# Kernel optimization log

Measured on AMD Instinct MI355X. Metric: run time of the kernel, lower is better.

The kernel has to match this reference:

```python
import jax, jax.numpy as jnp
import numpy as np

EPS = 1e-5
N0, K1, K2 = 1000, 500, 100  # node counts fixed by the view() calls in the source


def _conv_bn_relu(x, w, b, g, be):
    # Conv1d(k=1) == per-node linear; BatchNorm1d in training mode over nodes
    h = x @ w.T + b                      # (N, Cout)
    mu = h.mean(0)
    var = h.var(0)                       # biased variance, as torch BN uses
    return jax.nn.relu(g * (h - mu) * jax.lax.rsqrt(var + EPS) + be)


def _linear_relu(x, w, b):
    return jax.nn.relu(x @ w.T + b)


def _sag_pool(x, src, dst, ew, w_rel, w_root, bias, k):
    # SAGPooling with GraphConv scorer (sum aggregation weighted by edge_attr)
    N = x.shape[0]
    agg = jax.ops.segment_sum(ew[:, None] * x[src], dst, num_segments=N)  # (N, C)
    score = agg @ w_rel + x @ w_root + bias                               # (N,)
    top_s, perm = jax.lax.top_k(score, k)
    xk = x[perm] * jnp.tanh(top_s)[:, None]                               # (k, C)
    # re-index edges: keep only edges between surviving nodes (mask, fixed E)
    new_idx = jnp.zeros(N, jnp.int32).at[perm].set(jnp.arange(k, dtype=jnp.int32))
    keep = jnp.zeros(N, bool).at[perm].set(True)
    valid = keep[src] & keep[dst]
    nsrc = jnp.where(valid, new_idx[src], 0)
    ndst = jnp.where(valid, new_idx[dst], 0)
    new_ew = jnp.where(valid, ew, 0.0)  # zero weight == edge removed
    return xk, nsrc, ndst, new_ew


def setup_inputs() -> dict:
    key = jax.random.key(0)
    ks = jax.random.split(key, 32)
    nrm = lambda k, sh, s=0.05: jax.random.normal(k, sh, jnp.float32) * s
    E = 32000
    return {
        "x": jax.random.normal(ks[0], (1, N0, 3), jnp.float32),
        "edge_index": jax.random.randint(ks[1], (2, E), 0, N0, jnp.int32),
        "edge_attr": jax.random.uniform(ks[2], (E,), jnp.float32),
        # input: Conv1d(3,64)+BN
        "w0": nrm(ks[3], (64, 3)), "b0": jnp.zeros(64), "g0": jnp.ones(64), "be0": jnp.zeros(64),
        # mlp_first: Conv1d(64,64)+BN
        "w1": nrm(ks[4], (64, 64)), "b1": jnp.zeros(64), "g1": jnp.ones(64), "be1": jnp.zeros(64),
        # mlp_second: Conv1d(64,128)+BN, Conv1d(128,200)+BN
        "w2a": nrm(ks[5], (128, 64)), "b2a": jnp.zeros(128), "g2a": jnp.ones(128), "be2a": jnp.zeros(128),
        "w2b": nrm(ks[6], (200, 128)), "b2b": jnp.zeros(200), "g2b": jnp.ones(200), "be2b": jnp.zeros(200),
        # mlp_third: Conv1d(200,128), Conv1d(128,2) (no BN)
        "w3a": nrm(ks[7], (128, 200)), "b3a": jnp.zeros(128),
        "w3b": nrm(ks[8], (2, 128)), "b3b": jnp.zeros(2),
        # SAGPooling scorers (GraphConv(in_channels, 1))
        "p1_wrel": nrm(ks[9], (64,)), "p1_wroot": nrm(ks[10], (64,)), "p1_b": jnp.zeros(()),
        "p2_wrel": nrm(ks[11], (200,)), "p2_wroot": nrm(ks[12], (200,)), "p2_b": jnp.zeros(()),
    }


def reference(x, edge_index, edge_attr,
              w0, b0, g0, be0, w1, b1, g1, be1,
              w2a, b2a, g2a, be2a, w2b, b2b, g2b, be2b,
              w3a, b3a, w3b, b3b,
              p1_wrel, p1_wroot, p1_b, p2_wrel, p2_wroot, p2_b):
    h = x.reshape(N0, 3)
    src, dst = edge_index[0], edge_index[1]
    ew = edge_attr.reshape(-1)

    h = _conv_bn_relu(h, w0, b0, g0, be0)      # (1000, 64)
    h = _conv_bn_relu(h, w1, b1, g1, be1)      # (1000, 64)
    h, src, dst, ew = _sag_pool(h, src, dst, ew, p1_wrel, p1_wroot, p1_b, K1)

    h = _conv_bn_relu(h, w2a, b2a, g2a, be2a)  # (500, 128)
    h = _conv_bn_relu(h, w2b, b2b, g2b, be2b)  # (500, 200)
    h, src, dst, ew = _sag_pool(h, src, dst, ew, p2_wrel, p2_wroot, p2_b, K2)

    g = h.max(0)                               # global max pool over 100 nodes -> (200,)
    h3 = _linear_relu(g, w3a, b3a)             # (128,)
    out = _linear_relu(h3, w3b, b3b)           # (2,)
    return jax.nn.log_softmax(out)[None, :]    # (1, 2)
```

## Files before the change

kernel.cpp:

```cpp
#include <hip/hip_runtime.h>
#include <math.h>

#define EPS 1e-5f
#define N0 1000
#define K1 500
#define K2 100
#define NE 32000

__device__ __forceinline__ float bnr(float h, float sc, float sh) {
    float v = fmaf(h, sc, sh);
    return v > 0.f ? v : 0.f;
}

__global__ void k_lin0(const float* __restrict__ x, const float* __restrict__ w0,
                       const float* __restrict__ b0, float* __restrict__ h0,
                       float* __restrict__ psum0) {
    int t = threadIdx.x;
    int c = t & 63, ns = t >> 6;
    int nb = blockIdx.x * 128;
    float wa = w0[c * 3 + 0], wb = w0[c * 3 + 1], wc = w0[c * 3 + 2], bb = b0[c];
    float s = 0.f, q = 0.f;
    for (int j = 0; j < 32; ++j) {
        int n = nb + ns + 4 * j;
        if (n < N0) {
            float h = fmaf(wa, x[n * 3], fmaf(wb, x[n * 3 + 1], fmaf(wc, x[n * 3 + 2], bb)));
            h0[n * 64 + c] = h;
            s += h; q += h * h;
        }
    }
    __shared__ float rs[256], rq[256];
    rs[t] = s; rq[t] = q;
    __syncthreads();
    if (ns == 0) {
        psum0[blockIdx.x * 128 + c]      = rs[c] + rs[c + 64] + rs[c + 128] + rs[c + 192];
        psum0[blockIdx.x * 128 + 64 + c] = rq[c] + rq[c + 64] + rq[c + 128] + rq[c + 192];
    }
}

__global__ void k_lin1(const float* __restrict__ h0, const float* __restrict__ w1,
                       const float* __restrict__ b1v, const float* __restrict__ g0,
                       const float* __restrict__ be0, const float* __restrict__ psum0,
                       float* __restrict__ h1, float* __restrict__ psum1) {
    __shared__ float xs[64][65];
    __shared__ float wsm[64][65];
    __shared__ float sc0[64], sh0[64];
    __shared__ float rs[256], rq[256];
    int t = threadIdx.x;
    int nb = blockIdx.x * 64;
    if (t < 64) {
        float s = 0.f, q = 0.f;
        for (int i = 0; i < 8; ++i) { s += psum0[i * 128 + t]; q += psum0[i * 128 + 64 + t]; }
        float mu = s * (1.f / N0);
        float var = q * (1.f / N0) - mu * mu;
        float sc = g0[t] * rsqrtf(var + EPS);
        sc0[t] = sc; sh0[t] = be0[t] - mu * sc;
    }
    __syncthreads();
    for (int i = 0; i < 16; ++i) {
        int e = t + i * 256;
        int r = e >> 6, cc = e & 63;
        int n = nb + r;
        xs[r][cc] = (n < N0) ? bnr(h0[n * 64 + cc], sc0[cc], sh0[cc]) : 0.f;
        wsm[r][cc] = w1[e];
    }
    __syncthreads();
    int c = t & 63, ns = t >> 6;
    float s = 0.f, q = 0.f;
    for (int j = 0; j < 16; ++j) {
        int ln = ns + 4 * j;
        int n = nb + ln;
        if (n < N0) {
            float acc = b1v[c];
            #pragma unroll
            for (int k = 0; k < 64; ++k) acc = fmaf(xs[ln][k], wsm[c][k], acc);
            h1[n * 64 + c] = acc;
            s += acc; q += acc * acc;
        }
    }
    rs[t] = s; rq[t] = q;
    __syncthreads();
    if (ns == 0) {
        psum1[blockIdx.x * 128 + c]      = rs[c] + rs[c + 64] + rs[c + 128] + rs[c + 192];
        psum1[blockIdx.x * 128 + 64 + c] = rq[c] + rq[c + 64] + rq[c + 128] + rq[c + 192];
    }
}

__global__ void k_score1(const float* __restrict__ h1, const float* __restrict__ psum1,
                         const float* __restrict__ g1, const float* __restrict__ be1,
                         const float* __restrict__ wrel, const float* __restrict__ wroot,
                         const float* __restrict__ pb,
                         float* __restrict__ t1, float* __restrict__ sc1) {
    __shared__ float sc[64], sh[64];
    int t = threadIdx.x;
    if (t < 64) {
        float s = 0.f, q = 0.f;
        for (int i = 0; i < 16; ++i) { s += psum1[i * 128 + t]; q += psum1[i * 128 + 64 + t]; }
        float mu = s * (1.f / N0);
        float var = q * (1.f / N0) - mu * mu;
        float sv = g1[t] * rsqrtf(var + EPS);
        sc[t] = sv; sh[t] = be1[t] - mu * sv;
    }
    __syncthreads();
    int lane = t & 63, w = t >> 6;
    int n = blockIdx.x * 4 + w;
    if (n < N0) {
        float v = bnr(h1[n * 64 + lane], sc[lane], sh[lane]);
        float dr = v * wrel[lane], dt = v * wroot[lane];
        #pragma unroll
        for (int m = 32; m >= 1; m >>= 1) {
            dr += __shfl_xor(dr, m, 64);
            dt += __shfl_xor(dt, m, 64);
        }
        if (lane == 0) { t1[n] = dr; sc1[n] = dt + pb[0]; }
    }
}

__global__ void k_scatter1(const int* __restrict__ ei, const float* __restrict__ ea,
                           const float* __restrict__ t1, float* __restrict__ sc1) {
    __shared__ float acc[N0];
    int t = threadIdx.x;
    for (int i = t; i < N0; i += 256) acc[i] = 0.f;
    __syncthreads();
    for (int e = blockIdx.x * 256 + t; e < NE; e += gridDim.x * 256) {
        float w = ea[e];
        if (w != 0.f) atomicAdd(&acc[ei[NE + e]], w * t1[ei[e]]);
    }
    __syncthreads();
    for (int i = t; i < N0; i += 256) {
        float v = acc[i];
        if (v != 0.f) atomicAdd(&sc1[i], v);
    }
}

__global__ void k_rank1(const float* __restrict__ sc1, const float* __restrict__ h1,
                        const float* __restrict__ psum1, const float* __restrict__ g1,
                        const float* __restrict__ be1,
                        float* __restrict__ xp1, int* __restrict__ keep, int* __restrict__ nidx) {
    __shared__ float ss[N0];
    __shared__ float sc[64], sh[64];
    int t = threadIdx.x;
    if (t < 64) {
        float s = 0.f, q = 0.f;
        for (int i = 0; i < 16; ++i) { s += psum1[i * 128 + t]; q += psum1[i * 128 + 64 + t]; }
        float mu = s * (1.f / N0);
        float var = q * (1.f / N0) - mu * mu;
        float sv = g1[t] * rsqrtf(var + EPS);
        sc[t] = sv; sh[t] = be1[t] - mu * sv;
    }
    for (int i = t; i < N0; i += 256) ss[i] = sc1[i];
    __syncthreads();
    int lane = t & 63, w = t >> 6;
    int n = blockIdx.x * 4 + w;
    if (n < N0) {
        float s = ss[n];
        int r = 0;
        for (int m = lane; m < N0; m += 64) {
            float sm = ss[m];
            r += (sm > s) || (sm == s && m < n);
        }
        #pragma unroll
        for (int msk = 32; msk >= 1; msk >>= 1) r += __shfl_xor(r, msk, 64);
        if (lane == 0) { keep[n] = (r < K1) ? 1 : 0; nidx[n] = (r < K1) ? r : 0; }
        if (r < K1) {
            float tn = tanhf(s);
            xp1[r * 64 + lane] = bnr(h1[n * 64 + lane], sc[lane], sh[lane]) * tn;
        }
    }
}

__global__ void k_lin2a_remap(const float* __restrict__ xp1, const float* __restrict__ w2a,
                              const float* __restrict__ b2a, float* __restrict__ h2a,
                              float* __restrict__ psum2a,
                              const int* __restrict__ ei, const float* __restrict__ ea,
                              const int* __restrict__ keep, const int* __restrict__ nidx,
                              int* __restrict__ nsrc, int* __restrict__ ndst,
                              float* __restrict__ new_ew) {
    __shared__ float xs[64][65];
    __shared__ float wsm[128][65];
    __shared__ float rs[256], rq[256];
    int b = blockIdx.x;
    int t = threadIdx.x;
    if (b < 8) {
        int nb = b * 64;
        for (int i = 0; i < 16; ++i) {
            int e = t + i * 256;
            int r = e >> 6, cc = e & 63;
            int n = nb + r;
            xs[r][cc] = (n < K1) ? xp1[n * 64 + cc] : 0.f;
        }
        for (int i = 0; i < 32; ++i) {
            int e = t + i * 256;
            wsm[e >> 6][e & 63] = w2a[e];
        }
        __syncthreads();
        int c = t & 127, ns = t >> 7;
        float s = 0.f, q = 0.f;
        for (int j = 0; j < 32; ++j) {
            int ln = ns + 2 * j;
            int n = nb + ln;
            if (n < K1) {
                float acc = b2a[c];
                #pragma unroll
                for (int k = 0; k < 64; ++k) acc = fmaf(xs[ln][k], wsm[c][k], acc);
                h2a[n * 128 + c] = acc;
                s += acc; q += acc * acc;
            }
        }
        rs[t] = s; rq[t] = q;
        __syncthreads();
        if (ns == 0) {
            psum2a[b * 256 + c]       = rs[c] + rs[c + 128];
            psum2a[b * 256 + 128 + c] = rq[c] + rq[c + 128];
        }
    } else {
        int e = (b - 8) * 256 + t;
        if (e < NE) {
            int s = ei[e], d = ei[NE + e];
            bool v = keep[s] && keep[d];
            nsrc[e] = v ? nidx[s] : 0;
            ndst[e] = v ? nidx[d] : 0;
            new_ew[e] = v ? ea[e] : 0.f;
        }
    }
}

__global__ void k_lin2b(const float* __restrict__ h2a, const float* __restrict__ psum2a,
                        const float* __restrict__ g2a, const float* __restrict__ be2a,
                        const float* __restrict__ w2b, const float* __restrict__ b2b,
                        float* __restrict__ h2b, float* __restrict__ psum2b) {
    __shared__ float wsm[200][33];
    __shared__ float xs[25][33];
    __shared__ float sc[128], sh[128];
    int t = threadIdx.x;
    if (t < 128) {
        float s = 0.f, q = 0.f;
        for (int i = 0; i < 8; ++i) { s += psum2a[i * 256 + t]; q += psum2a[i * 256 + 128 + t]; }
        float mu = s * (1.f / K1);
        float var = q * (1.f / K1) - mu * mu;
        float sv = g2a[t] * rsqrtf(var + EPS);
        sc[t] = sv; sh[t] = be2a[t] - mu * sv;
    }
    __syncthreads();
    int nb = blockIdx.x * 25;
    float acc[25];
    if (t < 200) {
        float bb = b2b[t];
        #pragma unroll
        for (int r = 0; r < 25; ++r) acc[r] = bb;
    }
    for (int kt = 0; kt < 4; ++kt) {
        int k0 = kt * 32;
        __syncthreads();
        for (int e = t; e < 200 * 32; e += 256) {
            int r = e >> 5, k = e & 31;
            wsm[r][k] = w2b[r * 128 + k0 + k];
        }
        for (int e = t; e < 25 * 32; e += 256) {
            int r = e >> 5, k = e & 31;
            int n = nb + r;
            xs[r][k] = bnr(h2a[n * 128 + k0 + k], sc[k0 + k], sh[k0 + k]);
        }
        __syncthreads();
        if (t < 200) {
            for (int k = 0; k < 32; ++k) {
                float wv = wsm[t][k];
                #pragma unroll
                for (int r = 0; r < 25; ++r) acc[r] = fmaf(xs[r][k], wv, acc[r]);
            }
        }
    }
    if (t < 200) {
        float s = 0.f, q = 0.f;
        #pragma unroll
        for (int r = 0; r < 25; ++r) {
            int n = nb + r;
            h2b[n * 200 + t] = acc[r];
            s += acc[r]; q += acc[r] * acc[r];
        }
        psum2b[blockIdx.x * 400 + t]       = s;
        psum2b[blockIdx.x * 400 + 200 + t] = q;
    }
}

__global__ void k_score2(const float* __restrict__ h2b, const float* __restrict__ psum2b,
                         const float* __restrict__ g2b, const float* __restrict__ be2b,
                         const float* __restrict__ wrel, const float* __restrict__ wroot,
                         const float* __restrict__ pb,
                         float* __restrict__ t2, float* __restrict__ sc2) {
    __shared__ float sc[200], sh[200];
    int t = threadIdx.x;
    if (t < 200) {
        float s = 0.f, q = 0.f;
        for (int i = 0; i < 20; ++i) { s += psum2b[i * 400 + t]; q += psum2b[i * 400 + 200 + t]; }
        float mu = s * (1.f / K1);
        float var = q * (1.f / K1) - mu * mu;
        float sv = g2b[t] * rsqrtf(var + EPS);
        sc[t] = sv; sh[t] = be2b[t] - mu * sv;
    }
    __syncthreads();
    int lane = t & 63, w = t >> 6;
    int n = blockIdx.x * 4 + w;
    if (n < K1) {
        float dr = 0.f, dt = 0.f;
        #pragma unroll
        for (int j = 0; j < 4; ++j) {
            int ch = lane + 64 * j;
            if (ch < 200) {
                float v = bnr(h2b[n * 200 + ch], sc[ch], sh[ch]);
                dr = fmaf(v, wrel[ch], dr);
                dt = fmaf(v, wroot[ch], dt);
            }
        }
        #pragma unroll
        for (int m = 32; m >= 1; m >>= 1) {
            dr += __shfl_xor(dr, m, 64);
            dt += __shfl_xor(dt, m, 64);
        }
        if (lane == 0) { t2[n] = dr; sc2[n] = dt + pb[0]; }
    }
}

__global__ void k_scatter2(const int* __restrict__ nsrc, const int* __restrict__ ndst,
                           const float* __restrict__ new_ew, const float* __restrict__ t2,
                           float* __restrict__ sc2) {
    __shared__ float acc[K1];
    int t = threadIdx.x;
    for (int i = t; i < K1; i += 256) acc[i] = 0.f;
    __syncthreads();
    for (int e = blockIdx.x * 256 + t; e < NE; e += gridDim.x * 256) {
        float w = new_ew[e];
        if (w != 0.f) atomicAdd(&acc[ndst[e]], w * t2[nsrc[e]]);
    }
    __syncthreads();
    for (int i = t; i < K1; i += 256) {
        float v = acc[i];
        if (v != 0.f) atomicAdd(&sc2[i], v);
    }
}

__global__ void k_rank2(const float* __restrict__ sc2v, const float* __restrict__ h2b,
                        const float* __restrict__ psum2b, const float* __restrict__ g2b,
                        const float* __restrict__ be2b, float* __restrict__ xp2) {
    __shared__ float ss[K1];
    __shared__ float sc[200], sh[200];
    int t = threadIdx.x;
    if (t < 200) {
        float s = 0.f, q = 0.f;
        for (int i = 0; i < 20; ++i) { s += psum2b[i * 400 + t]; q += psum2b[i * 400 + 200 + t]; }
        float mu = s * (1.f / K1);
        float var = q * (1.f / K1) - mu * mu;
        float sv = g2b[t] * rsqrtf(var + EPS);
        sc[t] = sv; sh[t] = be2b[t] - mu * sv;
    }
    for (int i = t; i < K1; i += 256) ss[i] = sc2v[i];
    __syncthreads();
    int lane = t & 63, w = t >> 6;
    int n = blockIdx.x * 4 + w;
    if (n < K1) {
        float s = ss[n];
        int r = 0;
        for (int m = lane; m < K1; m += 64) {
            float sm = ss[m];
            r += (sm > s) || (sm == s && m < n);
        }
        #pragma unroll
        for (int msk = 32; msk >= 1; msk >>= 1) r += __shfl_xor(r, msk, 64);
        if (r < K2) {
            float tn = tanhf(s);
            #pragma unroll
            for (int j = 0; j < 4; ++j) {
                int ch = lane + 64 * j;
                if (ch < 200)
                    xp2[r * 200 + ch] = bnr(h2b[n * 200 + ch], sc[ch], sh[ch]) * tn;
            }
        }
    }
}

__global__ void k_final(const float* __restrict__ xp2, const float* __restrict__ w3a,
                        const float* __restrict__ b3a, const float* __restrict__ w3b,
                        const float* __restrict__ b3b, float* __restrict__ out) {
    __shared__ float g[200];
    __shared__ float buf[64][201];
    __shared__ float part[256];
    __shared__ float h3[128];
    __shared__ float o[2];
    int t = threadIdx.x;
    if (t < 200) {
        float m = -1e30f;
        for (int n = 0; n < K2; ++n) m = fmaxf(m, xp2[n * 200 + t]);
        g[t] = m;
    }
    __syncthreads();
    int lane = t & 63, q = t >> 6;
    for (int chunk = 0; chunk < 2; ++chunk) {
        int r0 = chunk * 64;
        __syncthreads();
        for (int e = t; e < 64 * 200; e += 256) {
            int r = e / 200, j = e - r * 200;
            buf[r][j] = w3a[r0 * 200 + e];
        }
        __syncthreads();
        float p = 0.f;
        for (int j = q * 50; j < q * 50 + 50; ++j) p = fmaf(buf[lane][j], g[j], p);
        part[t] = p;
        __syncthreads();
        if (t < 64) {
            float a = part[t] + part[t + 64] + part[t + 128] + part[t + 192] + b3a[r0 + t];
            h3[r0 + t] = fmaxf(a, 0.f);
        }
    }
    __syncthreads();
    if (t < 128) {
        int ow = t >> 6;
        float p = w3b[ow * 128 + lane] * h3[lane] + w3b[ow * 128 + 64 + lane] * h3[64 + lane];
        #pragma unroll
        for (int m = 32; m >= 1; m >>= 1) p += __shfl_xor(p, m, 64);
        if (lane == 0) o[ow] = fmaxf(p + b3b[ow], 0.f);
    }
    __syncthreads();
    if (t == 0) {
        float m = fmaxf(o[0], o[1]);
        float l = m + logf(expf(o[0] - m) + expf(o[1] - m));
        out[0] = o[0] - l;
        out[1] = o[1] - l;
    }
}

extern "C" void kernel_launch(void* const* d_in, const int* in_sizes, int n_in,
                              void* d_out, int out_size, void* d_ws, size_t ws_size,
                              hipStream_t stream) {
    const float* x    = (const float*)d_in[0];
    const int*   ei   = (const int*)d_in[1];
    const float* ea   = (const float*)d_in[2];
    const float* w0   = (const float*)d_in[3];
    const float* b0   = (const float*)d_in[4];
    const float* g0   = (const float*)d_in[5];
    const float* be0  = (const float*)d_in[6];
    const float* w1   = (const float*)d_in[7];
    const float* b1   = (const float*)d_in[8];
    const float* g1   = (const float*)d_in[9];
    const float* be1  = (const float*)d_in[10];
    const float* w2a  = (const float*)d_in[11];
    const float* b2a  = (const float*)d_in[12];
    const float* g2a  = (const float*)d_in[13];
    const float* be2a = (const float*)d_in[14];
    const float* w2b  = (const float*)d_in[15];
    const float* b2b  = (const float*)d_in[16];
    const float* g2b  = (const float*)d_in[17];
    const float* be2b = (const float*)d_in[18];
    const float* w3a  = (const float*)d_in[19];
    const float* b3a  = (const float*)d_in[20];
    const float* w3b  = (const float*)d_in[21];
    const float* b3b  = (const float*)d_in[22];
    const float* p1_wrel  = (const float*)d_in[23];
    const float* p1_wroot = (const float*)d_in[24];
    const float* p1_b     = (const float*)d_in[25];
    const float* p2_wrel  = (const float*)d_in[26];
    const float* p2_wroot = (const float*)d_in[27];
    const float* p2_b     = (const float*)d_in[28];

    float* ws = (float*)d_ws;
    float* h0     = ws;
    float* h1     = ws + 64000;
    float* psum0  = ws + 128000;
    float* psum1  = ws + 129024;
    float* psum2a = ws + 131072;
    float* psum2b = ws + 133120;
    float* t1     = ws + 141120;
    float* sc1    = ws + 142120;
    float* xp1    = ws + 143120;
    float* h2a    = ws + 175120;
    float* h2b    = ws + 239120;
    float* t2     = ws + 339120;
    float* sc2    = ws + 339620;
    float* xp2    = ws + 340120;
    int*   keep   = (int*)(ws + 360120);
    int*   nidx   = (int*)(ws + 361120);
    int*   nsrc   = (int*)(ws + 362120);
    int*   ndst   = (int*)(ws + 394120);
    float* new_ew = ws + 426120;

    float* out = (float*)d_out;

    k_lin0<<<8, 256, 0, stream>>>(x, w0, b0, h0, psum0);
    k_lin1<<<16, 256, 0, stream>>>(h0, w1, b1, g0, be0, psum0, h1, psum1);
    k_score1<<<250, 256, 0, stream>>>(h1, psum1, g1, be1, p1_wrel, p1_wroot, p1_b, t1, sc1);
    k_scatter1<<<16, 256, 0, stream>>>(ei, ea, t1, sc1);
    k_rank1<<<250, 256, 0, stream>>>(sc1, h1, psum1, g1, be1, xp1, keep, nidx);
    k_lin2a_remap<<<133, 256, 0, stream>>>(xp1, w2a, b2a, h2a, psum2a,
                                           ei, ea, keep, nidx, nsrc, ndst, new_ew);
    k_lin2b<<<20, 256, 0, stream>>>(h2a, psum2a, g2a, be2a, w2b, b2b, h2b, psum2b);
    k_score2<<<125, 256, 0, stream>>>(h2b, psum2b, g2b, be2b, p2_wrel, p2_wroot, p2_b, t2, sc2);
    k_scatter2<<<16, 256, 0, stream>>>(nsrc, ndst, new_ew, t2, sc2);
    k_rank2<<<125, 256, 0, stream>>>(sc2, h2b, psum2b, g2b, be2b, xp2);
    k_final<<<1, 256, 0, stream>>>(xp2, w3a, b3a, w3b, b3b, out);
}
```

Baseline: 130.3 us.

## Fuse all stages into one persistent kernel with software grid barriers

Replaces eleven separate kernel launches with a pre-clear kernel plus one persistent 64-block kernel. The stages are separated by an atomic generation-counter grid barrier, which is meant to remove per-launch overhead and the gaps between launches. BatchNorm partial sums now go into global accumulators through atomicAdd instead of per-block partial arrays. In exchange, each stage runs on at most 64 blocks, so wide stages like scoring and ranking lose parallelism. The spin barrier also relies on all 64 blocks being resident at the same time.

Result: slower. 171.7 us (+31.8%).

```diff
diff --git a/kernel.cpp b/kernel.cpp
--- a/kernel.cpp
+++ b/kernel.cpp
@@ -6,191 +6,206 @@
 #define K1 500
 #define K2 100
 #define NE 32000
+#define NB 64
 
 __device__ __forceinline__ float bnr(float h, float sc, float sh) {
     float v = fmaf(h, sc, sh);
     return v > 0.f ? v : 0.f;
 }
 
-__global__ void k_lin0(const float* __restrict__ x, const float* __restrict__ w0,
-                       const float* __restrict__ b0, float* __restrict__ h0,
-                       float* __restrict__ psum0) {
+struct Args {
+    const float *x; const int *ei; const float *ea;
+    const float *w0, *b0, *g0, *be0;
+    const float *w1, *b1, *g1, *be1;
+    const float *w2a, *b2a, *g2a, *be2a;
+    const float *w2b, *b2b, *g2b, *be2b;
+    const float *w3a, *b3a, *w3b, *b3b;
+    const float *p1_wrel, *p1_wroot, *p1_b, *p2_wrel, *p2_wroot, *p2_b;
+    float *h0, *h1, *sums0, *sums1, *sums2a, *sums2b;
+    float *t1, *sc1, *xp1, *h2a, *h2b, *t2, *sc2, *xp2;
+    int *keep, *nidx, *nsrc, *ndst; float *new_ew;
+    unsigned *bar, *gen;
+    float *out;
+};
+
+__device__ __forceinline__ void gsync(unsigned* bar, unsigned* gen) {
+    __syncthreads();
+    if (threadIdx.x == 0) {
+        unsigned g = __hip_atomic_load(gen, __ATOMIC_RELAXED, __HIP_MEMORY_SCOPE_AGENT);
+        unsigned a = __hip_atomic_fetch_add(bar, 1u, __ATOMIC_ACQ_REL, __HIP_MEMORY_SCOPE_AGENT);
+        if (a == NB - 1) {
+            __hip_atomic_store(bar, 0u, __ATOMIC_RELAXED, __HIP_MEMORY_SCOPE_AGENT);
+            __hip_atomic_fetch_add(gen, 1u, __ATOMIC_ACQ_REL, __HIP_MEMORY_SCOPE_AGENT);
+        } else {
+            while (__hip_atomic_load(gen, __ATOMIC_ACQUIRE, __HIP_MEMORY_SCOPE_AGENT) == g) {
+                __builtin_amdgcn_s_sleep(1);
+            }
+        }
+        __threadfence();
+    }
+    __syncthreads();
+}
+
+__global__ void k_pre(float* sums, unsigned* bar, unsigned* gen) {
     int t = threadIdx.x;
-    int c = t & 63, ns = t >> 6;
-    int nb = blockIdx.x * 128;
-    float wa = w0[c * 3 + 0], wb = w0[c * 3 + 1], wc = w0[c * 3 + 2], bb = b0[c];
-    float s = 0.f, q = 0.f;
-    for (int j = 0; j < 32; ++j) {
-        int n = nb + ns + 4 * j;
-        if (n < N0) {
-            float h = fmaf(wa, x[n * 3], fmaf(wb, x[n * 3 + 1], fmaf(wc, x[n * 3 + 2], bb)));
-            h0[n * 64 + c] = h;
-            s += h; q += h * h;
-        }
-    }
-    __shared__ float rs[256], rq[256];
-    rs[t] = s; rq[t] = q;
-    __syncthreads();
-    if (ns == 0) {
-        psum0[blockIdx.x * 128 + c]      = rs[c] + rs[c + 64] + rs[c + 128] + rs[c + 192];
-        psum0[blockIdx.x * 128 + 64 + c] = rq[c] + rq[c + 64] + rq[c + 128] + rq[c + 192];
-    }
+    for (int i = t; i < 912; i += 256) sums[i] = 0.f;
+    if (t == 0) { *bar = 0u; *gen = 0u; }
 }
 
-__global__ void k_lin1(const float* __restrict__ h0, const float* __restrict__ w1,
-                       const float* __restrict__ b1v, const float* __restrict__ g0,
-                       const float* __restrict__ be0, const float* __restrict__ psum0,
-                       float* __restrict__ h1, float* __restrict__ psum1) {
-    __shared__ float xs[64][65];
-    __shared__ float wsm[64][65];
-    __shared__ float sc0[64], sh0[64];
-    __shared__ float rs[256], rq[256];
-    int t = threadIdx.x;
-    int nb = blockIdx.x * 64;
-    if (t < 64) {
+__global__ __launch_bounds__(256) void k_mega(Args a) {
+    union SMem {
+        struct { float xs[64][65], wsm[128][65], rs[256], rq[256], sc[64], sh[64]; } mm;
+        struct { float wsm[200][33], xs[10][33], sc[128], sh[128]; } l2b;
+        struct { float acc[N0]; } sct;
+        struct { float ss[N0], sc[200], sh[200]; } rk;
+        struct { float sc[200], sh[200]; } bn;
+        struct { float g[200], h3[128], o[2]; } fin;
+    };
+    __shared__ SMem sm;
+    const int b = blockIdx.x, t = threadIdx.x;
+    const int lane = t & 63, wv = t >> 6;
+
+    if (b < 8) {
+        int c = lane, ns = wv;
+        int nb = b * 128;
+        float wa = a.w0[c * 3], wb = a.w0[c * 3 + 1], wc = a.w0[c * 3 + 2], bb = a.b0[c];
         float s = 0.f, q = 0.f;
-        for (int i = 0; i < 8; ++i) { s += psum0[i * 128 + t]; q += psum0[i * 128 + 64 + t]; }
-        float mu = s * (1.f / N0);
-        float var = q * (1.f / N0) - mu * mu;
-        float sc = g0[t] * rsqrtf(var + EPS);
-        sc0[t] = sc; sh0[t] = be0[t] - mu * sc;
-    }
-    __syncthreads();
-    for (int i = 0; i < 16; ++i) {
-        int e = t + i * 256;
-        int r = e >> 6, cc = e & 63;
-        int n = nb + r;
-        xs[r][cc] = (n < N0) ? bnr(h0[n * 64 + cc], sc0[cc], sh0[cc]) : 0.f;
-        wsm[r][cc] = w1[e];
-    }
-    __syncthreads();
-    int c = t & 63, ns = t >> 6;
-    float s = 0.f, q = 0.f;
-    for (int j = 0; j < 16; ++j) {
-        int ln = ns + 4 * j;
-        int n = nb + ln;
-        if (n < N0) {
-            float acc = b1v[c];
-            #pragma unroll
-            for (int k = 0; k < 64; ++k) acc = fmaf(xs[ln][k], wsm[c][k], acc);
-            h1[n * 64 + c] = acc;
-            s += acc; q += acc * acc;
-        }
-    }
-    rs[t] = s; rq[t] = q;
-    __syncthreads();
-    if (ns == 0) {
-        psum1[blockIdx.x * 128 + c]      = rs[c] + rs[c + 64] + rs[c + 128] + rs[c + 192];
-        psum1[blockIdx.x * 128 + 64 + c] = rq[c] + rq[c + 64] + rq[c + 128] + rq[c + 192];
-    }
-}
-
-__global__ void k_score1(const float* __restrict__ h1, const float* __restrict__ psum1,
-                         const float* __restrict__ g1, const float* __restrict__ be1,
-                         const float* __restrict__ wrel, const float* __restrict__ wroot,
-                         const float* __restrict__ pb,
-                         float* __restrict__ t1, float* __restrict__ sc1) {
-    __shared__ float sc[64], sh[64];
-    int t = threadIdx.x;
-    if (t < 64) {
+        for (int j = 0; j < 32; ++j) {
+            int n = nb + ns + 4 * j;
+            if (n < N0) {
+                float h = fmaf(wa, a.x[n * 3], fmaf(wb, a.x[n * 3 + 1], fmaf(wc, a.x[n * 3 + 2], bb)));
+                a.h0[n * 64 + c] = h;
+                s += h; q += h * h;
+            }
+        }
+        sm.mm.rs[t] = s; sm.mm.rq[t] = q;
+        __syncthreads();
+        if (ns == 0) {
+            atomicAdd(&a.sums0[c],      sm.mm.rs[c] + sm.mm.rs[c + 64] + sm.mm.rs[c + 128] + sm.mm.rs[c + 192]);
+            atomicAdd(&a.sums0[64 + c], sm.mm.rq[c] + sm.mm.rq[c + 64] + sm.mm.rq[c + 128] + sm.mm.rq[c + 192]);
+        }
+    }
+    gsync(a.bar, a.gen);
+
+    if (b < 16) {
+        int nb = b * 64;
+        if (t < 64) {
+            float mu = a.sums0[t] * (1.f / N0);
+            float var = a.sums0[64 + t] * (1.f / N0) - mu * mu;
+            float s = a.g0[t] * rsqrtf(var + EPS);
+            sm.mm.sc[t] = s; sm.mm.sh[t] = a.be0[t] - mu * s;
+        }
+        __syncthreads();
+        for (int i = 0; i < 16; ++i) {
+            int e = t + i * 256;
+            int r = e >> 6, cc = e & 63;
+            int n = nb + r;
+            sm.mm.xs[r][cc] = (n < N0) ? bnr(a.h0[n * 64 + cc], sm.mm.sc[cc], sm.mm.sh[cc]) : 0.f;
+            sm.mm.wsm[r][cc] = a.w1[e];
+        }
+        __syncthreads();
+        int c = lane, ns = wv;
         float s = 0.f, q = 0.f;
-        for (int i = 0; i < 16; ++i) { s += psum1[i * 128 + t]; q += psum1[i * 128 + 64 + t]; }
-        float mu = s * (1.f / N0);
-        float var = q * (1.f / N0) - mu * mu;
-        float sv = g1[t] * rsqrtf(var + EPS);
-        sc[t] = sv; sh[t] = be1[t] - mu * sv;
-    }
-    __syncthreads();
-    int lane = t & 63, w = t >> 6;
-    int n = blockIdx.x * 4 + w;
-    if (n < N0) {
-        float v = bnr(h1[n * 64 + lane], sc[lane], sh[lane]);
-        float dr = v * wrel[lane], dt = v * wroot[lane];
-        #pragma unroll
-        for (int m = 32; m >= 1; m >>= 1) {
-            dr += __shfl_xor(dr, m, 64);
-            dt += __shfl_xor(dt, m, 64);
-        }
-        if (lane == 0) { t1[n] = dr; sc1[n] = dt + pb[0]; }
-    }
-}
-
-__global__ void k_scatter1(const int* __restrict__ ei, const float* __restrict__ ea,
-                           const float* __restrict__ t1, float* __restrict__ sc1) {
-    __shared__ float acc[N0];
-    int t = threadIdx.x;
-    for (int i = t; i < N0; i += 256) acc[i] = 0.f;
-    __syncthreads();
-    for (int e = blockIdx.x * 256 + t; e < NE; e += gridDim.x * 256) {
-        float w = ea[e];
-        if (w != 0.f) atomicAdd(&acc[ei[NE + e]], w * t1[ei[e]]);
-    }
-    __syncthreads();
-    for (int i = t; i < N0; i += 256) {
-        float v = acc[i];
-        if (v != 0.f) atomicAdd(&sc1[i], v);
-    }
-}
-
-__global__ void k_rank1(const float* __restrict__ sc1, const float* __restrict__ h1,
-                        const float* __restrict__ psum1, const float* __restrict__ g1,
-                        const float* __restrict__ be1,
-                        float* __restrict__ xp1, int* __restrict__ keep, int* __restrict__ nidx) {
-    __shared__ float ss[N0];
-    __shared__ float sc[64], sh[64];
-    int t = threadIdx.x;
-    if (t < 64) {
-        float s = 0.f, q = 0.f;
-        for (int i = 0; i < 16; ++i) { s += psum1[i * 128 + t]; q += psum1[i * 128 + 64 + t]; }
-        float mu = s * (1.f / N0);
-        float var = q * (1.f / N0) - mu * mu;
-        float sv = g1[t] * rsqrtf(var + EPS);
-        sc[t] = sv; sh[t] = be1[t] - mu * sv;
-    }
-    for (int i = t; i < N0; i += 256) ss[i] = sc1[i];
-    __syncthreads();
-    int lane = t & 63, w = t >> 6;
-    int n = blockIdx.x * 4 + w;
-    if (n < N0) {
-        float s = ss[n];
-        int r = 0;
-        for (int m = lane; m < N0; m += 64) {
-            float sm = ss[m];
-            r += (sm > s) || (sm == s && m < n);
-        }
-        #pragma unroll
-        for (int msk = 32; msk >= 1; msk >>= 1) r += __shfl_xor(r, msk, 64);
-        if (lane == 0) { keep[n] = (r < K1) ? 1 : 0; nidx[n] = (r < K1) ? r : 0; }
-        if (r < K1) {
-            float tn = tanhf(s);
-            xp1[r * 64 + lane] = bnr(h1[n * 64 + lane], sc[lane], sh[lane]) * tn;
-        }
-    }
-}
-
-__global__ void k_lin2a_remap(const float* __restrict__ xp1, const float* __restrict__ w2a,
-                              const float* __restrict__ b2a, float* __restrict__ h2a,
-                              float* __restrict__ psum2a,
-                              const int* __restrict__ ei, const float* __restrict__ ea,
-                              const int* __restrict__ keep, const int* __restrict__ nidx,
-                              int* __restrict__ nsrc, int* __restrict__ ndst,
-                              float* __restrict__ new_ew) {
-    __shared__ float xs[64][65];
-    __shared__ float wsm[128][65];
-    __shared__ float rs[256], rq[256];
-    int b = blockIdx.x;
-    int t = threadIdx.x;
+        for (int j = 0; j < 16; ++j) {
+            int ln = ns + 4 * j;
+            int n = nb + ln;
+            if (n < N0) {
+                float acc = a.b1[c];
+                #pragma unroll
+                for (int k = 0; k < 64; ++k) acc = fmaf(sm.mm.xs[ln][k], sm.mm.wsm[c][k], acc);
+                a.h1[n * 64 + c] = acc;
+                s += acc; q += acc * acc;
+            }
+        }
+        sm.mm.rs[t] = s; sm.mm.rq[t] = q;
+        __syncthreads();
+        if (ns == 0) {
+            atomicAdd(&a.sums1[c],      sm.mm.rs[c] + sm.mm.rs[c + 64] + sm.mm.rs[c + 128] + sm.mm.rs[c + 192]);
+            atomicAdd(&a.sums1[64 + c], sm.mm.rq[c] + sm.mm.rq[c + 64] + sm.mm.rq[c + 128] + sm.mm.rq[c + 192]);
+        }
+    }
+    gsync(a.bar, a.gen);
+
+    if (b * 16 < N0) {
+        if (t < 64) {
+            float mu = a.sums1[t] * (1.f / N0);
+            float var = a.sums1[64 + t] * (1.f / N0) - mu * mu;
+            float sv = a.g1[t] * rsqrtf(var + EPS);
+            sm.bn.sc[t] = sv; sm.bn.sh[t] = a.be1[t] - mu * sv;
+        }
+        __syncthreads();
+        for (int it = 0; it < 4; ++it) {
+            int n = b * 16 + it * 4 + wv;
+            if (n < N0) {
+                float v = bnr(a.h1[n * 64 + lane], sm.bn.sc[lane], sm.bn.sh[lane]);
+                float dr = v * a.p1_wrel[lane], dt = v * a.p1_wroot[lane];
+                #pragma unroll
+                for (int m = 32; m >= 1; m >>= 1) {
+                    dr += __shfl_xor(dr, m, 64);
+                    dt += __shfl_xor(dt, m, 64);
+                }
+                if (lane == 0) { a.t1[n] = dr; a.sc1[n] = dt + a.p1_b[0]; }
+            }
+        }
+    }
+    gsync(a.bar, a.gen);
+
+    if (b < 16) {
+        for (int i = t; i < N0; i += 256) sm.sct.acc[i] = 0.f;
+        __syncthreads();
+        for (int e = b * 256 + t; e < NE; e += 16 * 256) {
+            float w = a.ea[e];
+            if (w != 0.f) atomicAdd(&sm.sct.acc[a.ei[NE + e]], w * a.t1[a.ei[e]]);
+        }
+        __syncthreads();
+        for (int i = t; i < N0; i += 256) {
+            float v = sm.sct.acc[i];
+            if (v != 0.f) atomicAdd(&a.sc1[i], v);
+        }
+    }
+    gsync(a.bar, a.gen);
+
+    if (b * 16 < N0) {
+        if (t < 64) {
+            float mu = a.sums1[t] * (1.f / N0);
+            float var = a.sums1[64 + t] * (1.f / N0) - mu * mu;
+            float sv = a.g1[t] * rsqrtf(var + EPS);
+            sm.rk.sc[t] = sv; sm.rk.sh[t] = a.be1[t] - mu * sv;
+        }
+        for (int i = t; i < N0; i += 256) sm.rk.ss[i] = a.sc1[i];
+        __syncthreads();
+        for (int it = 0; it < 4; ++it) {
+            int n = b * 16 + it * 4 + wv;
+            if (n < N0) {
+                float s = sm.rk.ss[n];
+                int r = 0;
+                for (int m = lane; m < N0; m += 64) {
+                    float smv = sm.rk.ss[m];
+                    r += (smv > s) || (smv == s && m < n);
+                }
+                #pragma unroll
+                for (int msk = 32; msk >= 1; msk >>= 1) r += __shfl_xor(r, msk, 64);
+                if (lane == 0) { a.keep[n] = (r < K1) ? 1 : 0; a.nidx[n] = (r < K1) ? r : 0; }
+                if (r < K1) {
+                    float tn = tanhf(s);
+                    a.xp1[r * 64 + lane] = bnr(a.h1[n * 64 + lane], sm.rk.sc[lane], sm.rk.sh[lane]) * tn;
+                }
+            }
+        }
+    }
+    gsync(a.bar, a.gen);
+
     if (b < 8) {
         int nb = b * 64;
         for (int i = 0; i < 16; ++i) {
             int e = t + i * 256;
             int r = e >> 6, cc = e & 63;
             int n = nb + r;
-            xs[r][cc] = (n < K1) ? xp1[n * 64 + cc] : 0.f;
+            sm.mm.xs[r][cc] = (n < K1) ? a.xp1[n * 64 + cc] : 0.f;
         }
         for (int i = 0; i < 32; ++i) {
             int e = t + i * 256;
-            wsm[e >> 6][e & 63] = w2a[e];
+            sm.mm.wsm[e >> 6][e & 63] = a.w2a[e];
         }
         __syncthreads();
         int c = t & 127, ns = t >> 7;
@@ -199,300 +214,249 @@
             int ln = ns + 2 * j;
             int n = nb + ln;
             if (n < K1) {
-                float acc = b2a[c];
-                #pragma unroll
-                for (int k = 0; k < 64; ++k) acc = fmaf(xs[ln][k], wsm[c][k], acc);
-                h2a[n * 128 + c] = acc;
+                float acc = a.b2a[c];
+                #pragma unroll
+                for (int k = 0; k < 64; ++k) acc = fmaf(sm.mm.xs[ln][k], sm.mm.wsm[c][k], acc);
+                a.h2a[n * 128 + c] = acc;
                 s += acc; q += acc * acc;
             }
         }
-        rs[t] = s; rq[t] = q;
+        sm.mm.rs[t] = s; sm.mm.rq[t] = q;
         __syncthreads();
         if (ns == 0) {
-            psum2a[b * 256 + c]       = rs[c] + rs[c + 128];
-            psum2a[b * 256 + 128 + c] = rq[c] + rq[c + 128];
+            atomicAdd(&a.sums2a[c],       sm.mm.rs[c] + sm.mm.rs[c + 128]);
+            atomicAdd(&a.sums2a[128 + c], sm.mm.rq[c] + sm.mm.rq[c + 128]);
         }
     } else {
-        int e = (b - 8) * 256 + t;
-        if (e < NE) {
-            int s = ei[e], d = ei[NE + e];
-            bool v = keep[s] && keep[d];
-            nsrc[e] = v ? nidx[s] : 0;
-            ndst[e] = v ? nidx[d] : 0;
-            new_ew[e] = v ? ea[e] : 0.f;
-        }
-    }
-}
-
-__global__ void k_lin2b(const float* __restrict__ h2a, const float* __restrict__ psum2a,
-                        const float* __restrict__ g2a, const float* __restrict__ be2a,
-                        const float* __restrict__ w2b, const float* __restrict__ b2b,
-                        float* __restrict__ h2b, float* __restrict__ psum2b) {
-    __shared__ float wsm[200][33];
-    __shared__ float xs[25][33];
-    __shared__ float sc[128], sh[128];
-    int t = threadIdx.x;
-    if (t < 128) {
-        float s = 0.f, q = 0.f;
-        for (int i = 0; i < 8; ++i) { s += psum2a[i * 256 + t]; q += psum2a[i * 256 + 128 + t]; }
-        float mu = s * (1.f / K1);
-        float var = q * (1.f / K1) - mu * mu;
-        float sv = g2a[t] * rsqrtf(var + EPS);
-        sc[t] = sv; sh[t] = be2a[t] - mu * sv;
-    }
-    __syncthreads();
-    int nb = blockIdx.x * 25;
-    float acc[25];
-    if (t < 200) {
-        float bb = b2b[t];
+        for (int e = (b - 8) * 256 + t; e < NE; e += 56 * 256) {
+            int s = a.ei[e], d = a.ei[NE + e];
+            bool v = a.keep[s] && a.keep[d];
+            a.nsrc[e] = v ? a.nidx[s] : 0;
+            a.ndst[e] = v ? a.nidx[d] : 0;
+            a.new_ew[e] = v ? a.ea[e] : 0.f;
+        }
+    }
+    gsync(a.bar, a.gen);
+
+    if (b < 50) {
+        if (t < 128) {
+            float mu = a.sums2a[t] * (1.f / K1);
+            float var = a.sums2a[128 + t] * (1.f / K1) - mu * mu;
+            float sv = a.g2a[t] * rsqrtf(var + EPS);
+            sm.l2b.sc[t] = sv; sm.l2b.sh[t] = a.be2a[t] - mu * sv;
+        }
+        __syncthreads();
+        int nb = b * 10;
+        float acc[10];
+        float bb = (t < 200) ? a.b2b[t] : 0.f;
         #pragma unroll
-        for (int r = 0; r < 25; ++r) acc[r] = bb;
-    }
-    for (int kt = 0; kt < 4; ++kt) {
-        int k0 = kt * 32;
-        __syncthreads();
-        for (int e = t; e < 200 * 32; e += 256) {
-            int r = e >> 5, k = e & 31;
-            wsm[r][k] = w2b[r * 128 + k0 + k];
-        }
-        for (int e = t; e < 25 * 32; e += 256) {
-            int r = e >> 5, k = e & 31;
-            int n = nb + r;
-            xs[r][k] = bnr(h2a[n * 128 + k0 + k], sc[k0 + k], sh[k0 + k]);
-        }
-        __syncthreads();
+        for (int r = 0; r < 10; ++r) acc[r] = bb;
+        for (int kt = 0; kt < 4; ++kt) {
+            int k0 = kt * 32;
+            __syncthreads();
+            for (int e = t; e < 200 * 32; e += 256) {
+                int r = e >> 5, k = e & 31;
+                sm.l2b.wsm[r][k] = a.w2b[r * 128 + k0 + k];
+            }
+            for (int e = t; e < 10 * 32; e += 256) {
+                int r = e >> 5, k = e & 31;
+                sm.l2b.xs[r][k] = bnr(a.h2a[(nb + r) * 128 + k0 + k], sm.l2b.sc[k0 + k], sm.l2b.sh[k0 + k]);
+            }
+            __syncthreads();
+            if (t < 200) {
+                for (int k = 0; k < 32; ++k) {
+                    float wv2 = sm.l2b.wsm[t][k];
+                    #pragma unroll
+                    for (int r = 0; r < 10; ++r) acc[r] = fmaf(sm.l2b.xs[r][k], wv2, acc[r]);
+                }
+            }
+        }
         if (t < 200) {
-            for (int k = 0; k < 32; ++k) {
-                float wv = wsm[t][k];
-                #pragma unroll
-                for (int r = 0; r < 25; ++r) acc[r] = fmaf(xs[r][k], wv, acc[r]);
-            }
-        }
-    }
-    if (t < 200) {
-        float s = 0.f, q = 0.f;
-        #pragma unroll
-        for (int r = 0; r < 25; ++r) {
-            int n = nb + r;
-            h2b[n * 200 + t] = acc[r];
-            s += acc[r]; q += acc[r] * acc[r];
-        }
-        psum2b[blockIdx.x * 400 + t]       = s;
-        psum2b[blockIdx.x * 400 + 200 + t] = q;
-    }
-}
-
-__global__ void k_score2(const float* __restrict__ h2b, const float* __restrict__ psum2b,
-                         const float* __restrict__ g2b, const float* __restrict__ be2b,
-                         const float* __restrict__ wrel, const float* __restrict__ wroot,
-                         const float* __restrict__ pb,
-                         float* __restrict__ t2, float* __restrict__ sc2) {
-    __shared__ float sc[200], sh[200];
-    int t = threadIdx.x;
-    if (t < 200) {
-        float s = 0.f, q = 0.f;
-        for (int i = 0; i < 20; ++i) { s += psum2b[i * 400 + t]; q += psum2b[i * 400 + 200 + t]; }
-        float mu = s * (1.f / K1);
-        float var = q * (1.f / K1) - mu * mu;
-        float sv = g2b[t] * rsqrtf(var + EPS);
-        sc[t] = sv; sh[t] = be2b[t] - mu * sv;
-    }
-    __syncthreads();
-    int lane = t & 63, w = t >> 6;
-    int n = blockIdx.x * 4 + w;
-    if (n < K1) {
-        float dr = 0.f, dt = 0.f;
-        #pragma unroll
-        for (int j = 0; j < 4; ++j) {
-            int ch = lane + 64 * j;
-            if (ch < 200) {
-                float v = bnr(h2b[n * 200 + ch], sc[ch], sh[ch]);
-                dr = fmaf(v, wrel[ch], dr);
-                dt = fmaf(v, wroot[ch], dt);
-            }
-        }
-        #pragma unroll
-        for (int m = 32; m >= 1; m >>= 1) {
-            dr += __shfl_xor(dr, m, 64);
-            dt += __shfl_xor(dt, m, 64);
-        }
-        if (lane == 0) { t2[n] = dr; sc2[n] = dt + pb[0]; }
-    }
-}
-
-__global__ void k_scatter2(const int* __restrict__ nsrc, const int* __restrict__ ndst,
-                           const float* __restrict__ new_ew, const float* __restrict__ t2,
-                           float* __restrict__ sc2) {
-    __shared__ float acc[K1];
-    int t = threadIdx.x;
-    for (int i = t; i < K1; i += 256) acc[i] = 0.f;
-    __syncthreads();
-    for (int e = blockIdx.x * 256 + t; e < NE; e += gridDim.x * 256) {
-        float w = new_ew[e];
-        if (w != 0.f) atomicAdd(&acc[ndst[e]], w * t2[nsrc[e]]);
-    }
-    __syncthreads();
-    for (int i = t; i < K1; i += 256) {
-        float v = acc[i];
-        if (v != 0.f) atomicAdd(&sc2[i], v);
-    }
-}
-
-__global__ void k_rank2(const float* __restrict__ sc2v, const float* __restrict__ h2b,
-                        const float* __restrict__ psum2b, const float* __restrict__ g2b,
-                        const float* __restrict__ be2b, float* __restrict__ xp2) {
-    __shared__ float ss[K1];
-    __shared__ float sc[200], sh[200];
-    int t = threadIdx.x;
-    if (t < 200) {
-        float s = 0.f, q = 0.f;
-        for (int i = 0; i < 20; ++i) { s += psum2b[i * 400 + t]; q += psum2b[i * 400 + 200 + t]; }
-        float mu = s * (1.f / K1);
-        float var = q * (1.f / K1) - mu * mu;
-        float sv = g2b[t] * rsqrtf(var + EPS);
-        sc[t] = sv; sh[t] = be2b[t] - mu * sv;
-    }
-    for (int i = t; i < K1; i += 256) ss[i] = sc2v[i];
-    __syncthreads();
-    int lane = t & 63, w = t >> 6;
-    int n = blockIdx.x * 4 + w;
-    if (n < K1) {
-        float s = ss[n];
-        int r = 0;
-        for (int m = lane; m < K1; m += 64) {
-            float sm = ss[m];
-            r += (sm > s) || (sm == s && m < n);
-        }
-        #pragma unroll
-        for (int msk = 32; msk >= 1; msk >>= 1) r += __shfl_xor(r, msk, 64);
-        if (r < K2) {
-            float tn = tanhf(s);
+            float s = 0.f, q = 0.f;
+            #pragma unroll
+            for (int r = 0; r < 10; ++r) {
+                a.h2b[(nb + r) * 200 + t] = acc[r];
+                s += acc[r]; q += acc[r] * acc[r];
+            }
+            atomicAdd(&a.sums2b[t], s);
+            atomicAdd(&a.sums2b[200 + t], q);
+        }
+    }
+    gsync(a.bar, a.gen);
+
+    if (b * 8 < K1) {
+        if (t < 200) {
+            float mu = a.sums2b[t] * (1.f / K1);
+            float var = a.sums2b[200 + t] * (1.f / K1) - mu * mu;
+            float sv = a.g2b[t] * rsqrtf(var + EPS);
+            sm.bn.sc[t] = sv; sm.bn.sh[t] = a.be2b[t] - mu * sv;
+        }
+        __syncthreads();
+        for (int it = 0; it < 2; ++it) {
+            int n = b * 8 + it * 4 + wv;
+            if (n < K1) {
+                float dr = 0.f, dt = 0.f;
+                #pragma unroll
+                for (int j = 0; j < 4; ++j) {
+                    int ch = lane + 64 * j;
+                    if (ch < 200) {
+                        float v = bnr(a.h2b[n * 200 + ch], sm.bn.sc[ch], sm.bn.sh[ch]);
+                        dr = fmaf(v, a.p2_wrel[ch], dr);
+                        dt = fmaf(v, a.p2_wroot[ch], dt);
+                    }
+                }
+                #pragma unroll
+                for (int m = 32; m >= 1; m >>= 1) {
+                    dr += __shfl_xor(dr, m, 64);
+                    dt += __shfl_xor(dt, m, 64);
+                }
+                if (lane == 0) { a.t2[n] = dr; a.sc2[n] = dt + a.p2_b[0]; }
+            }
+        }
+    }
+    gsync(a.bar, a.gen);
+
+    if (b < 16) {
+        for (int i = t; i < K1; i += 256) sm.sct.acc[i] = 0.f;
+        __syncthreads();
+        for (int e = b * 256 + t; e < NE; e += 16 * 256) {
+            float w = a.new_ew[e];
+            if (w != 0.f) atomicAdd(&sm.sct.acc[a.ndst[e]], w * a.t2[a.nsrc[e]]);
+        }
+        __syncthreads();
+        for (int i = t; i < K1; i += 256) {
+            float v = sm.sct.acc[i];
+            if (v != 0.f) atomicAdd(&a.sc2[i], v);
+        }
+    }
+    gsync(a.bar, a.gen);
+
+    if (b * 8 < K1) {
+        if (t < 200) {
+            float mu = a.sums2b[t] * (1.f / K1);
+            float var = a.sums2b[200 + t] * (1.f / K1) - mu * mu;
+            float sv = a.g2b[t] * rsqrtf(var + EPS);
+            sm.rk.sc[t] = sv; sm.rk.sh[t] = a.be2b[t] - mu * sv;
+        }
+        for (int i = t; i < K1; i += 256) sm.rk.ss[i] = a.sc2[i];
+        __syncthreads();
+        for (int it = 0; it < 2; ++it) {
+            int n = b * 8 + it * 4 + wv;
+            if (n < K1) {
+                float s = sm.rk.ss[n];
+                int r = 0;
+                for (int m = lane; m < K1; m += 64) {
+                    float smv = sm.rk.ss[m];
+                    r += (smv > s) || (smv == s && m < n);
+                }
+                #pragma unroll
+                for (int msk = 32; msk >= 1; msk >>= 1) r += __shfl_xor(r, msk, 64);
+                if (r < K2) {
+                    float tn = tanhf(s);
+                    #pragma unroll
+                    for (int j = 0; j < 4; ++j) {
+                        int ch = lane + 64 * j;
+                        if (ch < 200)
+                            a.xp2[r * 200 + ch] = bnr(a.h2b[n * 200 + ch], sm.rk.sc[ch], sm.rk.sh[ch]) * tn;
+                    }
+                }
+            }
+        }
+    }
+    gsync(a.bar, a.gen);
+
+    if (b == 0) {
+        if (t < 200) {
+            float m0 = -1e30f, m1 = -1e30f, m2 = -1e30f, m3 = -1e30f;
+            for (int n = 0; n < K2; n += 4) {
+                m0 = fmaxf(m0, a.xp2[n * 200 + t]);
+                m1 = fmaxf(m1, a.xp2[(n + 1) * 200 + t]);
+                m2 = fmaxf(m2, a.xp2[(n + 2) * 200 + t]);
+                m3 = fmaxf(m3, a.xp2[(n + 3) * 200 + t]);
+            }
+            sm.fin.g[t] = fmaxf(fmaxf(m0, m1), fmaxf(m2, m3));
+        }
+        __syncthreads();
+        for (int i = 0; i < 32; ++i) {
+            int r = wv + 4 * i;
+            float p = 0.f;
             #pragma unroll
             for (int j = 0; j < 4; ++j) {
                 int ch = lane + 64 * j;
-                if (ch < 200)
-                    xp2[r * 200 + ch] = bnr(h2b[n * 200 + ch], sc[ch], sh[ch]) * tn;
-            }
-        }
-    }
-}
-
-__global__ void k_final(const float* __restrict__ xp2, const float* __restrict__ w3a,
-                        const float* __restrict__ b3a, const float* __restrict__ w3b,
-                        const float* __restrict__ b3b, float* __restrict__ out) {
-    __shared__ float g[200];
-    __shared__ float buf[64][201];
-    __shared__ float part[256];
-    __shared__ float h3[128];
-    __shared__ float o[2];
-    int t = threadIdx.x;
-    if (t < 200) {
-        float m = -1e30f;
-        for (int n = 0; n < K2; ++n) m = fmaxf(m, xp2[n * 200 + t]);
-        g[t] = m;
-    }
-    __syncthreads();
-    int lane = t & 63, q = t >> 6;
-    for (int chunk = 0; chunk < 2; ++chunk) {
-        int r0 = chunk * 64;
-        __syncthreads();
-        for (int e = t; e < 64 * 200; e += 256) {
-            int r = e / 200, j = e - r * 200;
-            buf[r][j] = w3a[r0 * 200 + e];
-        }
-        __syncthreads();
-        float p = 0.f;
-        for (int j = q * 50; j < q * 50 + 50; ++j) p = fmaf(buf[lane][j], g[j], p);
-        part[t] = p;
-        __syncthreads();
-        if (t < 64) {
-            float a = part[t] + part[t + 64] + part[t + 128] + part[t + 192] + b3a[r0 + t];
-            h3[r0 + t] = fmaxf(a, 0.f);
-        }
-    }
-    __syncthreads();
-    if (t < 128) {
-        int ow = t >> 6;
-        float p = w3b[ow * 128 + lane] * h3[lane] + w3b[ow * 128 + 64 + lane] * h3[64 + lane];
-        #pragma unroll
-        for (int m = 32; m >= 1; m >>= 1) p += __shfl_xor(p, m, 64);
-        if (lane == 0) o[ow] = fmaxf(p + b3b[ow], 0.f);
-    }
-    __syncthreads();
-    if (t == 0) {
-        float m = fmaxf(o[0], o[1]);
-        float l = m + logf(expf(o[0] - m) + expf(o[1] - m));
-        out[0] = o[0] - l;
-        out[1] = o[1] - l;
+                if (ch < 200) p = fmaf(a.w3a[r * 200 + ch], sm.fin.g[ch], p);
+            }
+            #pragma unroll
+            for (int m = 32; m >= 1; m >>= 1) p += __shfl_xor(p, m, 64);
+            if (lane == 0) sm.fin.h3[r] = fmaxf(p + a.b3a[r], 0.f);
+        }
+        __syncthreads();
+        if (t < 128) {
+            int ow = t >> 6;
+            float p = a.w3b[ow * 128 + lane] * sm.fin.h3[lane]
+                    + a.w3b[ow * 128 + 64 + lane] * sm.fin.h3[64 + lane];
+            #pragma unroll
+            for (int m = 32; m >= 1; m >>= 1) p += __shfl_xor(p, m, 64);
+            if (lane == 0) sm.fin.o[ow] = fmaxf(p + a.b3b[ow], 0.f);
+        }
+        __syncthreads();
+        if (t == 0) {
+            float m = fmaxf(sm.fin.o[0], sm.fin.o[1]);
+            float l = m + logf(expf(sm.fin.o[0] - m) + expf(sm.fin.o[1] - m));
+            a.out[0] = sm.fin.o[0] - l;
+            a.out[1] = sm.fin.o[1] - l;
+        }
     }
 }
 
 extern "C" void kernel_launch(void* const* d_in, const int* in_sizes, int n_in,
                               void* d_out, int out_size, void* d_ws, size_t ws_size,
                               hipStream_t stream) {
-    const float* x    = (const float*)d_in[0];
-    const int*   ei   = (const int*)d_in[1];
-    const float* ea   = (const float*)d_in[2];
-    const float* w0   = (const float*)d_in[3];
-    const float* b0   = (const float*)d_in[4];
-    const float* g0   = (const float*)d_in[5];
-    const float* be0  = (const float*)d_in[6];
-    const float* w1   = (const float*)d_in[7];
-    const float* b1   = (const float*)d_in[8];
-    const float* g1   = (const float*)d_in[9];
-    const float* be1  = (const float*)d_in[10];
-    const float* w2a  = (const float*)d_in[11];
-    const float* b2a  = (const float*)d_in[12];
-    const float* g2a  = (const float*)d_in[13];
-    const float* be2a = (const float*)d_in[14];
-    const float* w2b  = (const float*)d_in[15];
-    const float* b2b  = (const float*)d_in[16];
-    const float* g2b  = (const float*)d_in[17];
-    const float* be2b = (const float*)d_in[18];
-    const float* w3a  = (const float*)d_in[19];
-    const float* b3a  = (const float*)d_in[20];
-    const float* w3b  = (const float*)d_in[21];
-    const float* b3b  = (const float*)d_in[22];
-    const float* p1_wrel  = (const float*)d_in[23];
-    const float* p1_wroot = (const float*)d_in[24];
-    const float* p1_b     = (const float*)d_in[25];
-    const float* p2_wrel  = (const float*)d_in[26];
-    const float* p2_wroot = (const float*)d_in[27];
-    const float* p2_b     = (const float*)d_in[28];
-
     float* ws = (float*)d_ws;
-    float* h0     = ws;
-    float* h1     = ws + 64000;
-    float* psum0  = ws + 128000;
-    float* psum1  = ws + 129024;
-    float* psum2a = ws + 131072;
-    float* psum2b = ws + 133120;
-    float* t1     = ws + 141120;
-    float* sc1    = ws + 142120;
-    float* xp1    = ws + 143120;
-    float* h2a    = ws + 175120;
-    float* h2b    = ws + 239120;
-    float* t2     = ws + 339120;
-    float* sc2    = ws + 339620;
-    float* xp2    = ws + 340120;
-    int*   keep   = (int*)(ws + 360120);
-    int*   nidx   = (int*)(ws + 361120);
-    int*   nsrc   = (int*)(ws + 362120);
-    int*   ndst   = (int*)(ws + 394120);
-    float* new_ew = ws + 426120;
-
-    float* out = (float*)d_out;
-
-    k_lin0<<<8, 256, 0, stream>>>(x, w0, b0, h0, psum0);
-    k_lin1<<<16, 256, 0, stream>>>(h0, w1, b1, g0, be0, psum0, h1, psum1);
-    k_score1<<<250, 256, 0, stream>>>(h1, psum1, g1, be1, p1_wrel, p1_wroot, p1_b, t1, sc1);
-    k_scatter1<<<16, 256, 0, stream>>>(ei, ea, t1, sc1);
-    k_rank1<<<250, 256, 0, stream>>>(sc1, h1, psum1, g1, be1, xp1, keep, nidx);
-    k_lin2a_remap<<<133, 256, 0, stream>>>(xp1, w2a, b2a, h2a, psum2a,
-                                           ei, ea, keep, nidx, nsrc, ndst, new_ew);
-    k_lin2b<<<20, 256, 0, stream>>>(h2a, psum2a, g2a, be2a, w2b, b2b, h2b, psum2b);
-    k_score2<<<125, 256, 0, stream>>>(h2b, psum2b, g2b, be2b, p2_wrel, p2_wroot, p2_b, t2, sc2);
-    k_scatter2<<<16, 256, 0, stream>>>(nsrc, ndst, new_ew, t2, sc2);
-    k_rank2<<<125, 256, 0, stream>>>(sc2, h2b, psum2b, g2b, be2b, xp2);
-    k_final<<<1, 256, 0, stream>>>(xp2, w3a, b3a, w3b, b3b, out);
+
+    Args a;
+    a.x    = (const float*)d_in[0];
+    a.ei   = (const int*)d_in[1];
+    a.ea   = (const float*)d_in[2];
+    a.w0   = (const float*)d_in[3];  a.b0   = (const float*)d_in[4];
+    a.g0   = (const float*)d_in[5];  a.be0  = (const float*)d_in[6];
+    a.w1   = (const float*)d_in[7];  a.b1   = (const float*)d_in[8];
+    a.g1   = (const float*)d_in[9];  a.be1  = (const float*)d_in[10];
+    a.w2a  = (const float*)d_in[11]; a.b2a  = (const float*)d_in[12];
+    a.g2a  = (const float*)d_in[13]; a.be2a = (const float*)d_in[14];
+    a.w2b  = (const float*)d_in[15]; a.b2b  = (const float*)d_in[16];
+    a.g2b  = (const float*)d_in[17]; a.be2b = (const float*)d_in[18];
+    a.w3a  = (const float*)d_in[19]; a.b3a  = (const float*)d_in[20];
+    a.w3b  = (const float*)d_in[21]; a.b3b  = (const float*)d_in[22];
+    a.p1_wrel  = (const float*)d_in[23];
+    a.p1_wroot = (const float*)d_in[24];
+    a.p1_b     = (const float*)d_in[25];
+    a.p2_wrel  = (const float*)d_in[26];
+    a.p2_wroot = (const float*)d_in[27];
+    a.p2_b     = (const float*)d_in[28];
+
+    a.h0     = ws;
+    a.h1     = ws + 64000;
+    a.sums0  = ws + 128000;
+    a.sums1  = ws + 128128;
+    a.sums2a = ws + 128256;
+    a.sums2b = ws + 128512;
+    a.t1     = ws + 129000;
+    a.sc1    = ws + 130000;
+    a.xp1    = ws + 131000;
+    a.h2a    = ws + 163000;
+    a.h2b    = ws + 227000;
+    a.t2     = ws + 327000;
+    a.sc2    = ws + 327500;
+    a.xp2    = ws + 328000;
+    a.keep   = (int*)(ws + 348000);
+    a.nidx   = (int*)(ws + 349000);
+    a.nsrc   = (int*)(ws + 350000);
+    a.ndst   = (int*)(ws + 382000);
+    a.new_ew = ws + 414000;
+    a.bar    = (unsigned*)(ws + 446080);
+    a.gen    = (unsigned*)(ws + 446144);
+    a.out    = (float*)d_out;
+
+    k_pre<<<1, 256, 0, stream>>>(a.sums0, a.bar, a.gen);
+    k_mega<<<NB, 256, 0, stream>>>(a);
 }
```
